# Optimization experiments

Measured on AMD Instinct MI355X. Metric: run time of the kernel, lower is better.

Reference implementation:

```python
import jax, jax.numpy as jnp
import numpy as np

T, B, E = 1024, 4, 1024
H = 16
D = E // H          # head_dim = 64
L = 16              # max_relative_length


def setup_inputs() -> dict:
    key = jax.random.key(0)
    ks = jax.random.split(key, 4)
    query = jax.random.normal(ks[0], (T, B, E), dtype=jnp.float32)
    # xavier-ish scaled params
    in_proj_weight = jax.random.normal(ks[1], (3 * E, E), dtype=jnp.float32) * (1.0 / np.sqrt(E))
    in_proj_bias = jnp.zeros((3 * E,), dtype=jnp.float32)
    rel_pos_keys = jax.random.normal(ks[2], (2 * L + 1, E), dtype=jnp.float32) * (1.0 / np.sqrt(E))
    out_w = jax.random.normal(ks[3], (E, E), dtype=jnp.float32) * (1.0 / np.sqrt(E))
    out_b = jnp.zeros((E,), dtype=jnp.float32)
    return {"query": query, "in_proj_weight": in_proj_weight, "in_proj_bias": in_proj_bias,
            "rel_pos_keys": rel_pos_keys, "out_w": out_w, "out_b": out_b}


def reference(query, in_proj_weight, in_proj_bias, rel_pos_keys, out_w, out_b):
    t, b, e = query.shape
    scaling = D ** (-0.5)
    # fused qkv projection: [T,B,3E]
    qkv = jnp.einsum('tbe,fe->tbf', query, in_proj_weight) + in_proj_bias
    q, k, v = jnp.split(qkv, 3, axis=-1)
    q = q * scaling
    # [T,B,E] -> [B*H, T, D]
    def heads(x):
        return x.reshape(t, b * H, D).transpose(1, 0, 2)
    q, k, v = heads(q), heads(k), heads(v)
    # clipped relative position matrix [T,T] in [0, 2L]
    r = jnp.arange(t)
    dist = jnp.clip(r[None, :] - r[:, None], -L, L) + L
    # gather relation keys, keep first head_dim channels: [T,T,D]
    rel_k = rel_pos_keys[dist][:, :, :D]
    # scores = q k^T + q . rel_k  (Shaw et al.), [B*H, T, T]
    scores = jnp.einsum('btd,bsd->bts', q, k) + jnp.einsum('btd,tsd->bts', q, rel_k)
    probs = jax.nn.softmax(scores, axis=-1)
    attn = jnp.einsum('bts,bsd->btd', probs, v)      # [B*H, T, D]
    attn = attn.transpose(1, 0, 2).reshape(t, b, e)   # [T, B, E]
    return jnp.einsum('tbe,oe->tbo', attn, out_w) + out_b
```

## Files before the change

kernel.cpp:

```cpp
#include <hip/hip_runtime.h>
#include <hip/hip_bf16.h>

typedef __attribute__((ext_vector_type(8))) short short8;
typedef __attribute__((ext_vector_type(4))) float floatx4;


#define QSCALE 0.18033688011112043f

__device__ __forceinline__ short f2bf(float x) {
  union { float f; unsigned u; } cv; cv.f = x;
  unsigned u = cv.u + (0x7FFFu + ((cv.u >> 16) & 1u));
  return (short)(u >> 16);
}

__device__ __forceinline__ unsigned pk_bf16(float a, float b) {
  union { __hip_bfloat162 h; unsigned u; } cv;
  cv.h = __float22bfloat162_rn(make_float2(a, b));
  return cv.u;
}

__device__ __forceinline__ float exp2_hw(float x) {
  return __builtin_amdgcn_exp2f(x);
}

__device__ __forceinline__ floatx4 mfma16(short8 a, short8 b, floatx4 c) {
  return __builtin_amdgcn_mfma_f32_16x16x32_bf16(a, b, c, 0, 0, 0);
}

__device__ __forceinline__ void async_copy16(const void* g, void* l) {
  __builtin_amdgcn_global_load_lds((const __attribute__((address_space(1))) void*)g,
                                   (__attribute__((address_space(3))) void*)l, 16, 0, 0);
}

__global__ void __launch_bounds__(256) convert_all_kernel(
    const float* __restrict__ s0, const float* __restrict__ s1,
    const float* __restrict__ s2,
    short* __restrict__ d0, short* __restrict__ d1, short* __restrict__ d2)
{
  int i = blockIdx.x * 256 + threadIdx.x;
  if (i < 524288) {
    int e8 = i & 127, b = (i >> 7) & 3, t = i >> 9;
    const float4* s = (const float4*)s0 + (size_t)i * 2;
    float4 a = s[0], c = s[1];
    uint4 o = make_uint4(pk_bf16(a.x, a.y), pk_bf16(a.z, a.w),
                         pk_bf16(c.x, c.y), pk_bf16(c.z, c.w));
    *(uint4*)(d0 + (size_t)b * 1048576 + t * 1024 + e8 * 8) = o;
  } else {
    const float* src; short* dst; int off;
    if (i < 917504) { src = s1; dst = d1; off = i - 524288; }
    else            { src = s2; dst = d2; off = i - 917504; }
    const float4* s = (const float4*)src + (size_t)off * 2;
    float4 a = s[0], c = s[1];
    uint4 o = make_uint4(pk_bf16(a.x, a.y), pk_bf16(a.z, a.w),
                         pk_bf16(c.x, c.y), pk_bf16(c.z, c.w));
    *(uint4*)(dst + (size_t)off * 8) = o;
  }
}

__device__ __forceinline__ void gemm_stage(
    const short* __restrict__ A, const short* __restrict__ W,
    short* Atile, short* Btile, int m0, int n0, int K, int kk, int tid, int w)
{
  #pragma unroll
  for (int i = 0; i < 2; i++) {
    int seg = i * 256 + tid;
    int row = seg >> 2, p = seg & 3;
    int ck = (p - ((row >> 1) & 3)) & 3;
    async_copy16(A + (size_t)(m0 + row) * K + kk + ck * 8,
                 Atile + (size_t)(i * 256 + w * 64) * 8);
    async_copy16(W + (size_t)(n0 + row) * K + kk + ck * 8,
                 Btile + (size_t)(i * 256 + w * 64) * 8);
  }
}

__device__ __forceinline__ void gemm_core_db(
    const short* __restrict__ A, const short* __restrict__ W,
    short* At, short* Bt,
    int m0, int n0, int K, int tid, floatx4 acc[4][4])
{
  const int lane = tid & 63, w = tid >> 6;
  const int quad = lane >> 4, l16 = lane & 15;
  const int wm = (w >> 1) * 64, wn = (w & 1) * 64;
  #pragma unroll
  for (int mt = 0; mt < 4; mt++)
    #pragma unroll
    for (int nt = 0; nt < 4; nt++) acc[mt][nt] = (floatx4)(0.0f);

  gemm_stage(A, W, At, Bt, m0, n0, K, 0, tid, w);

  for (int kk = 0; kk < K; kk += 32) {
    const int cur = (kk >> 5) & 1;
    short* Ac = At + cur * (128 * 32);
    short* Bc = Bt + cur * (128 * 32);
    __syncthreads();
    if (kk + 32 < K)
      gemm_stage(A, W, At + (1 - cur) * (128 * 32), Bt + (1 - cur) * (128 * 32),
                 m0, n0, K, kk + 32, tid, w);
    short8 af[4], bfr[4];
    #pragma unroll
    for (int mt = 0; mt < 4; mt++) {
      int R = wm + mt * 16 + l16;
      af[mt] = *(const short8*)(Ac + R * 32 + ((quad + (R >> 1)) & 3) * 8);
    }
    #pragma unroll
    for (int nt = 0; nt < 4; nt++) {
      int R = wn + nt * 16 + l16;
      bfr[nt] = *(const short8*)(Bc + R * 32 + ((quad + (R >> 1)) & 3) * 8);
    }
    #pragma unroll
    for (int mt = 0; mt < 4; mt++)
      #pragma unroll
      for (int nt = 0; nt < 4; nt++)
        acc[mt][nt] = mfma16(af[mt], bfr[nt], acc[mt][nt]);
  }
}

__global__ void __launch_bounds__(256) gemm_qkv(
    const short* __restrict__ A, const short* __restrict__ W,
    const float* __restrict__ bias,
    short* __restrict__ q_ws, short* __restrict__ k_ws, short* __restrict__ v_ws)
{
  __shared__ __align__(16) short Atile[2 * 128 * 32];
  __shared__ __align__(16) short Btile[2 * 128 * 32];
  const int tid = threadIdx.x;
  const int m0 = blockIdx.x * 128, n0 = blockIdx.y * 128;
  floatx4 acc[4][4];
  gemm_core_db(A, W, Atile, Btile, m0, n0, 1024, tid, acc);

  const int lane = tid & 63, w = tid >> 6;
  const int quad = lane >> 4, l16 = lane & 15;
  const int wm = (w >> 1) * 64, wn = (w & 1) * 64;
  const int which = n0 >> 10;
  #pragma unroll
  for (int nt = 0; nt < 4; nt++) {
    int f = n0 + wn + nt * 16 + l16;
    float bv = bias[f];
    int h = (f >> 6) & 15;
    int d = f & 63;
    if (which == 2) {
      #pragma unroll
      for (int mt = 0; mt < 4; mt++) {
        int r0 = m0 + wm + mt * 16 + quad * 4;
        int t = r0 & 1023, bb = r0 >> 10;
        int bh = bb * 16 + h;
        unsigned lo = pk_bf16(acc[mt][nt][0] + bv, acc[mt][nt][1] + bv);
        unsigned hi = pk_bf16(acc[mt][nt][2] + bv, acc[mt][nt][3] + bv);
        *(uint2*)(v_ws + ((size_t)bh * 64 + d) * 1024 + t) = make_uint2(lo, hi);
      }
    } else {
      short* dst = which ? k_ws : q_ws;
      const float sc = which ? 1.0f : QSCALE;
      #pragma unroll
      for (int mt = 0; mt < 4; mt++) {
        int r0 = m0 + wm + mt * 16 + quad * 4;
        int t = r0 & 1023, bb = r0 >> 10;
        int bh = bb * 16 + h;
        unsigned u01 = pk_bf16((acc[mt][nt][0] + bv) * sc, (acc[mt][nt][1] + bv) * sc);
        unsigned u23 = pk_bf16((acc[mt][nt][2] + bv) * sc, (acc[mt][nt][3] + bv) * sc);
        size_t base = ((size_t)bh * 1024 + t) * 64 + d;
        dst[base]           = (short)u01;
        dst[base + 64]      = (short)(u01 >> 16);
        dst[base + 128]     = (short)u23;
        dst[base + 192]     = (short)(u23 >> 16);
      }
    }
  }
}

__global__ void __launch_bounds__(256) attn_kernel(
    const short* __restrict__ q_ws, const short* __restrict__ k_ws,
    const short* __restrict__ v_ws, const float* __restrict__ relk,
    short* __restrict__ attn_ws)
{
  __shared__ float rel_lds[128 * 33];
  __shared__ __align__(16) short Ktile[2][64 * 64];
  __shared__ __align__(16) short Vtile[2][64 * 64];
  __shared__ __align__(16) short p_lds[4][32 * 64];
  const int tid = threadIdx.x, lane = tid & 63, w = tid >> 6;
  const int quad = lane >> 4, l16 = lane & 15;
  const int bh = 8 * ((int)blockIdx.x & 7) + (((int)blockIdx.x >> 3) & 7);
  const int t0 = ((int)blockIdx.x >> 6) * 128;
  const int b = bh >> 4, h = bh & 15;

  short8 aq[2][2];
  #pragma unroll
  for (int qt = 0; qt < 2; qt++)
    #pragma unroll
    for (int ks = 0; ks < 2; ks++)
      aq[qt][ks] = *(const short8*)(q_ws
          + ((size_t)bh * 1024 + t0 + qt * 64 + w * 16 + l16) * 64
          + ks * 32 + quad * 8);

  for (int i = tid; i < 48 * 8; i += 256) {
    int row = i >> 3, p = i & 7;
    short8 val;
    if (row < 33) {
      const float* src = relk + row * 1024 + p * 8;
      float4 a = *(const float4*)src, c = *(const float4*)(src + 4);
      val[0] = f2bf(a.x); val[1] = f2bf(a.y); val[2] = f2bf(a.z); val[3] = f2bf(a.w);
      val[4] = f2bf(c.x); val[5] = f2bf(c.y); val[6] = f2bf(c.z); val[7] = f2bf(c.w);
    } else {
      val = (short8)0;
    }
    *(short8*)(Ktile[0] + row * 64 + ((p ^ (row & 7)) << 3)) = val;
  }
  __syncthreads();

  #pragma unroll
  for (int qt = 0; qt < 2; qt++) {
    #pragma unroll
    for (int jt = 0; jt < 3; jt++) {
      floatx4 scR = (floatx4)(0.0f);
      #pragma unroll
      for (int ks = 0; ks < 2; ks++) {
        int rrow = jt * 16 + l16;
        int ck = (quad + 4 * ks) ^ (rrow & 7);
        short8 rb = *(const short8*)(Ktile[0] + rrow * 64 + ck * 8);
        scR = mfma16(aq[qt][ks], rb, scR);
      }
      int j = jt * 16 + l16;
      if (j < 33) {
        #pragma unroll
        for (int reg = 0; reg < 4; reg++) {
          int tl = qt * 64 + w * 16 + quad * 4 + reg;
          rel_lds[tl * 33 + j] = scR[reg];
        }
      }
    }
  }
  __syncthreads();

  float biasLo[2], biasHi[2];
  #pragma unroll
  for (int qt = 0; qt < 2; qt++) {
    int ql = qt * 64 + w * 16 + l16;
    biasLo[qt] = rel_lds[ql * 33 + 0];
    biasHi[qt] = rel_lds[ql * 33 + 32];
  }

  floatx4 o[2][4];
  #pragma unroll
  for (int qt = 0; qt < 2; qt++)
    #pragma unroll
    for (int dt = 0; dt < 4; dt++) o[qt][dt] = (floatx4)(0.0f);
  float rsum[2] = {0.f, 0.f};

  const short* kg = k_ws + (size_t)bh * 1024 * 64;
  const short* vg = v_ws + (size_t)bh * 64 * 1024;

  #define STAGE_KV(S0, BUF)                                                  \
    {                                                                        \
      _Pragma("unroll")                                                      \
      for (int i = 0; i < 2; i++) {                                          \
        int seg = i * 256 + tid;                                             \
        int row = seg >> 3, p = seg & 7;                                     \
        int ck = p ^ (row & 7);                                              \
        async_copy16(kg + (size_t)((S0) + row) * 64 + ck * 8,                \
                     Ktile[BUF] + (size_t)(i * 256 + w * 64) * 8);           \
        async_copy16(vg + (size_t)row * 1024 + (S0) + ck * 8,                \
                     Vtile[BUF] + (size_t)(i * 256 + w * 64) * 8);           \
      }                                                                      \
    }

  STAGE_KV(0, 0);

  for (int st = 0; st < 16; st++) {
    const int s0 = st * 64;
    const int cur = st & 1;
    __syncthreads();
    if (st < 15) STAGE_KV(s0 + 64, 1 - cur);

    short8 kb[4][2];
    #pragma unroll
    for (int nt = 0; nt < 4; nt++)
      #pragma unroll
      for (int ks = 0; ks < 2; ks++) {
        int srow = nt * 16 + l16;
        kb[nt][ks] = *(const short8*)(Ktile[cur] + srow * 64
                                      + (((quad + 4 * ks) ^ (l16 & 7)) << 3));
      }

    floatx4 sc[2][4];
    #pragma unroll
    for (int qt = 0; qt < 2; qt++)
      #pragma unroll
      for (int nt = 0; nt < 4; nt++) {
        sc[qt][nt] = (floatx4)(0.0f);
        #pragma unroll
        for (int ks = 0; ks < 2; ks++)
          sc[qt][nt] = mfma16(kb[nt][ks], aq[qt][ks], sc[qt][nt]);
      }

    #pragma unroll
    for (int qt = 0; qt < 2; qt++) {
      const int qbase = t0 + qt * 64 + w * 16;
      bool alllo = (s0 <= qbase - 79);
      bool allhi = (s0 >= qbase + 31);
      if (alllo || allhi) {
        float bb = alllo ? biasLo[qt] : biasHi[qt];
        #pragma unroll
        for (int nt = 0; nt < 4; nt++)
          #pragma unroll
          for (int reg = 0; reg < 4; reg++) sc[qt][nt][reg] += bb;
      } else {
        int ql = qt * 64 + w * 16 + l16;
        #pragma unroll
        for (int nt = 0; nt < 4; nt++)
          #pragma unroll
          for (int reg = 0; reg < 4; reg++) {
            int delta = (s0 + 16 * nt + 4 * quad + reg) - (qbase + l16);
            delta = min(max(delta, -16), 16) + 16;
            sc[qt][nt][reg] += rel_lds[ql * 33 + delta];
          }
      }
      #pragma unroll
      for (int nt = 0; nt < 4; nt++) {
        #pragma unroll
        for (int reg = 0; reg < 4; reg++) {
          float p = exp2_hw(sc[qt][nt][reg]);
          sc[qt][nt][reg] = p;
          rsum[qt] += p;
        }
        unsigned w0 = pk_bf16(sc[qt][nt][0], sc[qt][nt][1]);
        unsigned w1 = pk_bf16(sc[qt][nt][2], sc[qt][nt][3]);
        int srot = (16 * nt + 4 * quad + 4 * l16) & 63;
        *(uint2*)(p_lds[w] + (qt * 16 + l16) * 64 + srot) = make_uint2(w0, w1);
      }
    }

    short8 ap[2][2];
    #pragma unroll
    for (int qt = 0; qt < 2; qt++)
      #pragma unroll
      for (int ks = 0; ks < 2; ks++) {
        int s1 = (32 * ks + 8 * quad + 4 * l16) & 63;
        int s2 = (s1 + 4) & 63;
        union { short8 v; uint2 u[2]; } pu;
        pu.u[0] = *(const uint2*)(p_lds[w] + (qt * 16 + l16) * 64 + s1);
        pu.u[1] = *(const uint2*)(p_lds[w] + (qt * 16 + l16) * 64 + s2);
        ap[qt][ks] = pu.v;
      }

    #pragma unroll
    for (int dt = 0; dt < 4; dt++) {
      short8 vb[2];
      #pragma unroll
      for (int ks = 0; ks < 2; ks++) {
        int drow = dt * 16 + l16;
        vb[ks] = *(const short8*)(Vtile[cur] + drow * 64
                                  + (((quad + 4 * ks) ^ (l16 & 7)) << 3));
      }
      #pragma unroll
      for (int qt = 0; qt < 2; qt++)
        #pragma unroll
        for (int ks = 0; ks < 2; ks++)
          o[qt][dt] = mfma16(ap[qt][ks], vb[ks], o[qt][dt]);
    }
  }
  #undef STAGE_KV

  #pragma unroll
  for (int qt = 0; qt < 2; qt++) {
    float rs = rsum[qt];
    rs += __shfl_xor(rs, 16, 64);
    rs += __shfl_xor(rs, 32, 64);
    float inv[4];
    #pragma unroll
    for (int reg = 0; reg < 4; reg++)
      inv[reg] = 1.0f / __shfl(rs, quad * 4 + reg, 64);
    #pragma unroll
    for (int dt = 0; dt < 4; dt++) {
      unsigned u01 = pk_bf16(o[qt][dt][0] * inv[0], o[qt][dt][1] * inv[1]);
      unsigned u23 = pk_bf16(o[qt][dt][2] * inv[2], o[qt][dt][3] * inv[3]);
      int tg = t0 + qt * 64 + w * 16 + quad * 4;
      size_t base = ((size_t)tg * 4 + b) * 1024 + h * 64 + dt * 16 + l16;
      attn_ws[base]         = (short)u01;
      attn_ws[base + 4096]  = (short)(u01 >> 16);
      attn_ws[base + 8192]  = (short)u23;
      attn_ws[base + 12288] = (short)(u23 >> 16);
    }
  }
}

__global__ void __launch_bounds__(256) gemm_outproj(
    const short* __restrict__ A, const short* __restrict__ W,
    const float* __restrict__ bias, float* __restrict__ out)
{
  __shared__ __align__(16) short Atile[2 * 64 * 32];
  __shared__ __align__(16) short Btile[2 * 128 * 32];
  const int tid = threadIdx.x;
  const int m0 = blockIdx.x * 64, n0 = blockIdx.y * 128;
  const int lane = tid & 63, w = tid >> 6;
  const int quad = lane >> 4, l16 = lane & 15;
  const int wm = (w >> 1) * 32, wn = (w & 1) * 64;

  floatx4 acc[2][4];
  #pragma unroll
  for (int mt = 0; mt < 2; mt++)
    #pragma unroll
    for (int nt = 0; nt < 4; nt++) acc[mt][nt] = (floatx4)(0.0f);

  #define STAGE_OP(KK, BUF)                                                  \
    {                                                                        \
      _Pragma("unroll")                                                      \
      for (int i = 0; i < 2; i++) {                                          \
        int seg = i * 256 + tid;                \
        int row = seg >> 2, p = seg & 3;                                     \
        int ck = (p - ((row >> 1) & 3)) & 3;                                 \
        async_copy16(W + (size_t)(n0 + row) * 1024 + (KK) + ck * 8,          \
                     Btile + (size_t)((BUF) * 4096 + (i * 256 + w * 64) * 8)); \
      }                                                                      \
      {                                                                      \
        int row = tid >> 2, p = tid & 3;         \
        int ck = (p - ((row >> 1) & 3)) & 3;                                 \
        async_copy16(A + (size_t)(m0 + row) * 1024 + (KK) + ck * 8,          \
                     Atile + (size_t)((BUF) * 2048 + (w * 64) * 8));         \
      }                                                                      \
    }

  STAGE_OP(0, 0);
  for (int kk = 0; kk < 1024; kk += 32) {
    const int cur = (kk >> 5) & 1;
    const short* Ac = Atile + cur * 2048;
    const short* Bc = Btile + cur * 4096;
    __syncthreads();
    if (kk + 32 < 1024) STAGE_OP(kk + 32, 1 - cur);
    short8 af[2], bfr[4];
    #pragma unroll
    for (int mt = 0; mt < 2; mt++) {
      int R = wm + mt * 16 + l16;
      af[mt] = *(const short8*)(Ac + R * 32 + ((quad + (R >> 1)) & 3) * 8);
    }
    #pragma unroll
    for (int nt = 0; nt < 4; nt++) {
      int R = wn + nt * 16 + l16;
      bfr[nt] = *(const short8*)(Bc + R * 32 + ((quad + (R >> 1)) & 3) * 8);
    }
    #pragma unroll
    for (int mt = 0; mt < 2; mt++)
      #pragma unroll
      for (int nt = 0; nt < 4; nt++)
        acc[mt][nt] = mfma16(af[mt], bfr[nt], acc[mt][nt]);
  }
  #undef STAGE_OP

  #pragma unroll
  for (int nt = 0; nt < 4; nt++) {
    int f = n0 + wn + nt * 16 + l16;
    float bv = bias[f];
    #pragma unroll
    for (int mt = 0; mt < 2; mt++) {
      #pragma unroll
      for (int reg = 0; reg < 4; reg++) {
        int r = m0 + wm + mt * 16 + quad * 4 + reg;
        out[(size_t)r * 1024 + f] = acc[mt][nt][reg] + bv;
      }
    }
  }
}

extern "C" void kernel_launch(void* const* d_in, const int* in_sizes, int n_in,
                              void* d_out, int out_size, void* d_ws, size_t ws_size,
                              hipStream_t stream) {
  const float* query = (const float*)d_in[0];
  const float* in_w  = (const float*)d_in[1];
  const float* in_b  = (const float*)d_in[2];
  const float* relk  = (const float*)d_in[3];
  const float* out_w = (const float*)d_in[4];
  const float* out_b = (const float*)d_in[5];
  float* out = (float*)d_out;

  short* qry_bf = (short*)d_ws;
  short* win_bf = qry_bf + (size_t)4096 * 1024;
  short* wout_bf = win_bf + (size_t)3072 * 1024;
  short* q_ws   = wout_bf + (size_t)1024 * 1024;
  short* k_ws   = q_ws + (size_t)64 * 1024 * 64;
  short* v_ws   = k_ws + (size_t)64 * 1024 * 64;
  short* att_ws = v_ws + (size_t)64 * 1024 * 64;

  convert_all_kernel<<<4096, 256, 0, stream>>>(query, in_w, out_w,
                                               qry_bf, win_bf, wout_bf);
  gemm_qkv<<<dim3(32, 24), 256, 0, stream>>>(qry_bf, win_bf, in_b, q_ws, k_ws, v_ws);
  attn_kernel<<<512, 256, 0, stream>>>(q_ws, k_ws, v_ws, relk, att_ws);
  gemm_outproj<<<dim3(64, 8), 256, 0, stream>>>(att_ws, wout_bf, out_b, out);
}
```

Baseline: 175.4 us.

## Rewrite QKV GEMM with 256x256 tiles and ping-pong scheduled MFMA phases

The QKV projection GEMM moves from 128x128 tiles with 4 waves and K=32 stages to 256x256 tiles with 8 waves and K=64 stages. It uses XOR-swizzled LDS and a four-phase schedule per k-step that interleaves LDS fragment reads, async global loads and MFMA bursts. Barriers, sched_barrier and setprio pin that ordering. The aim is more data reuse per load and overlapping memory traffic with matrix math. The grid drops to 192 blocks, which leaves some CUs idle and uses much more LDS per block.

```diff
diff --git a/kernel.cpp b/kernel.cpp
--- a/kernel.cpp
+++ b/kernel.cpp
@@ -57,79 +57,162 @@
   }
 }
 
-__device__ __forceinline__ void gemm_stage(
-    const short* __restrict__ A, const short* __restrict__ W,
-    short* Atile, short* Btile, int m0, int n0, int K, int kk, int tid, int w)
-{
+__device__ __forceinline__ void stage_half8(const short* __restrict__ g,
+                                            short* l, int tid, int w) {
   #pragma unroll
   for (int i = 0; i < 2; i++) {
-    int seg = i * 256 + tid;
-    int row = seg >> 2, p = seg & 3;
-    int ck = (p - ((row >> 1) & 3)) & 3;
-    async_copy16(A + (size_t)(m0 + row) * K + kk + ck * 8,
-                 Atile + (size_t)(i * 256 + w * 64) * 8);
-    async_copy16(W + (size_t)(n0 + row) * K + kk + ck * 8,
-                 Btile + (size_t)(i * 256 + w * 64) * 8);
-  }
-}
-
-__device__ __forceinline__ void gemm_core_db(
-    const short* __restrict__ A, const short* __restrict__ W,
-    short* At, short* Bt,
-    int m0, int n0, int K, int tid, floatx4 acc[4][4])
-{
-  const int lane = tid & 63, w = tid >> 6;
-  const int quad = lane >> 4, l16 = lane & 15;
-  const int wm = (w >> 1) * 64, wn = (w & 1) * 64;
-  #pragma unroll
-  for (int mt = 0; mt < 4; mt++)
-    #pragma unroll
-    for (int nt = 0; nt < 4; nt++) acc[mt][nt] = (floatx4)(0.0f);
-
-  gemm_stage(A, W, At, Bt, m0, n0, K, 0, tid, w);
-
-  for (int kk = 0; kk < K; kk += 32) {
-    const int cur = (kk >> 5) & 1;
-    short* Ac = At + cur * (128 * 32);
-    short* Bc = Bt + cur * (128 * 32);
-    __syncthreads();
-    if (kk + 32 < K)
-      gemm_stage(A, W, At + (1 - cur) * (128 * 32), Bt + (1 - cur) * (128 * 32),
-                 m0, n0, K, kk + 32, tid, w);
-    short8 af[4], bfr[4];
-    #pragma unroll
-    for (int mt = 0; mt < 4; mt++) {
-      int R = wm + mt * 16 + l16;
-      af[mt] = *(const short8*)(Ac + R * 32 + ((quad + (R >> 1)) & 3) * 8);
-    }
-    #pragma unroll
-    for (int nt = 0; nt < 4; nt++) {
-      int R = wn + nt * 16 + l16;
-      bfr[nt] = *(const short8*)(Bc + R * 32 + ((quad + (R >> 1)) & 3) * 8);
-    }
-    #pragma unroll
-    for (int mt = 0; mt < 4; mt++)
-      #pragma unroll
-      for (int nt = 0; nt < 4; nt++)
-        acc[mt][nt] = mfma16(af[mt], bfr[nt], acc[mt][nt]);
-  }
-}
-
-__global__ void __launch_bounds__(256) gemm_qkv(
+    int seg = i * 512 + tid;
+    int row = seg >> 3, p = seg & 7;
+    int ck = p ^ (row & 7);
+    async_copy16(g + (size_t)row * 1024 + ck * 8,
+                 l + (size_t)(i * 512 + w * 64) * 8);
+  }
+}
+
+__global__ void __launch_bounds__(512, 2) gemm_qkv(
     const short* __restrict__ A, const short* __restrict__ W,
     const float* __restrict__ bias,
     short* __restrict__ q_ws, short* __restrict__ k_ws, short* __restrict__ v_ws)
 {
-  __shared__ __align__(16) short Atile[2 * 128 * 32];
-  __shared__ __align__(16) short Btile[2 * 128 * 32];
-  const int tid = threadIdx.x;
-  const int m0 = blockIdx.x * 128, n0 = blockIdx.y * 128;
-  floatx4 acc[4][4];
-  gemm_core_db(A, W, Atile, Btile, m0, n0, 1024, tid, acc);
-
-  const int lane = tid & 63, w = tid >> 6;
+  __shared__ __align__(16) short Atile[2 * 2 * 128 * 64];
+  __shared__ __align__(16) short Btile[2 * 2 * 128 * 64];
+  const int tid = threadIdx.x, lane = tid & 63, w = tid >> 6;
   const int quad = lane >> 4, l16 = lane & 15;
-  const int wm = (w >> 1) * 64, wn = (w & 1) * 64;
+  const int m0 = blockIdx.x * 256, n0 = blockIdx.y * 256;
+  const int wm = (w >> 2) * 128, wn = (w & 3) * 64;
+  const int rowB0 = (w & 1) * 64;
+
+  const short* Ag = A + (size_t)m0 * 1024;
+  const short* Wg = W + (size_t)n0 * 1024;
+
+  floatx4 acc[8][4];
+  #pragma unroll
+  for (int mt = 0; mt < 8; mt++)
+    #pragma unroll
+    for (int nt = 0; nt < 4; nt++) acc[mt][nt] = (floatx4)(0.0f);
+
+  #define SH_A(kc, h, buf) stage_half8(Ag + (size_t)(h) * 131072 + (kc) * 64, \
+                                       Atile + (buf) * 16384 + (h) * 8192, tid, w)
+  #define SH_B(kc, h, buf) stage_half8(Wg + (size_t)(h) * 131072 + (kc) * 64, \
+                                       Btile + (buf) * 16384 + (h) * 8192, tid, w)
+
+  SH_A(0, 0, 0); SH_A(0, 1, 0); SH_B(0, 0, 0); SH_B(0, 1, 0);
+  SH_A(1, 0, 1); SH_A(1, 1, 1);
+  asm volatile("s_waitcnt vmcnt(4)" ::: "memory");
+  __builtin_amdgcn_s_barrier();
+  asm volatile("" ::: "memory");
+
+  for (int kt = 0; kt < 16; ++kt) {
+    const int cur = kt & 1, nxt = cur ^ 1;
+    const short* Ah = Atile + cur * 16384 + (w >> 2) * 8192;
+    const short* Bh = Btile + cur * 16384 + ((w & 3) >> 1) * 8192;
+    const int kc1 = (kt + 1 < 16) ? kt + 1 : 15;
+    const int kc2 = (kt + 2 < 16) ? kt + 2 : 15;
+
+    short8 alo[4][2], ahi[4][2], blo[2][2], bhi[2][2];
+
+    #pragma unroll
+    for (int mt = 0; mt < 4; mt++) {
+      int r = mt * 16 + l16;
+      #pragma unroll
+      for (int ks = 0; ks < 2; ks++)
+        alo[mt][ks] = *(const short8*)(Ah + r * 64 + (((quad + 4 * ks) ^ (r & 7)) << 3));
+    }
+    #pragma unroll
+    for (int nt = 0; nt < 2; nt++) {
+      int r = rowB0 + nt * 16 + l16;
+      #pragma unroll
+      for (int ks = 0; ks < 2; ks++)
+        blo[nt][ks] = *(const short8*)(Bh + r * 64 + (((quad + 4 * ks) ^ (r & 7)) << 3));
+    }
+    SH_B(kc1, 0, nxt);
+    asm volatile("" ::: "memory");
+    __builtin_amdgcn_s_barrier();
+    __builtin_amdgcn_sched_barrier(0);
+    __builtin_amdgcn_s_setprio(1);
+    #pragma unroll
+    for (int mt = 0; mt < 4; mt++)
+      #pragma unroll
+      for (int nt = 0; nt < 2; nt++)
+        #pragma unroll
+        for (int ks = 0; ks < 2; ks++)
+          acc[mt][nt] = mfma16(alo[mt][ks], blo[nt][ks], acc[mt][nt]);
+    __builtin_amdgcn_s_setprio(0);
+    __builtin_amdgcn_sched_barrier(0);
+    __builtin_amdgcn_s_barrier();
+    asm volatile("" ::: "memory");
+
+    #pragma unroll
+    for (int mt = 0; mt < 4; mt++) {
+      int r = 64 + mt * 16 + l16;
+      #pragma unroll
+      for (int ks = 0; ks < 2; ks++)
+        ahi[mt][ks] = *(const short8*)(Ah + r * 64 + (((quad + 4 * ks) ^ (r & 7)) << 3));
+    }
+    SH_B(kc1, 1, nxt);
+    asm volatile("" ::: "memory");
+    __builtin_amdgcn_s_barrier();
+    __builtin_amdgcn_sched_barrier(0);
+    __builtin_amdgcn_s_setprio(1);
+    #pragma unroll
+    for (int mt = 0; mt < 4; mt++)
+      #pragma unroll
+      for (int nt = 0; nt < 2; nt++)
+        #pragma unroll
+        for (int ks = 0; ks < 2; ks++)
+          acc[4 + mt][nt] = mfma16(ahi[mt][ks], blo[nt][ks], acc[4 + mt][nt]);
+    __builtin_amdgcn_s_setprio(0);
+    __builtin_amdgcn_sched_barrier(0);
+    __builtin_amdgcn_s_barrier();
+    asm volatile("" ::: "memory");
+
+    #pragma unroll
+    for (int nt = 0; nt < 2; nt++) {
+      int r = rowB0 + (2 + nt) * 16 + l16;
+      #pragma unroll
+      for (int ks = 0; ks < 2; ks++)
+        bhi[nt][ks] = *(const short8*)(Bh + r * 64 + (((quad + 4 * ks) ^ (r & 7)) << 3));
+    }
+    SH_A(kc2, 0, cur);
+    asm volatile("" ::: "memory");
+    __builtin_amdgcn_s_barrier();
+    __builtin_amdgcn_sched_barrier(0);
+    __builtin_amdgcn_s_setprio(1);
+    #pragma unroll
+    for (int mt = 0; mt < 4; mt++)
+      #pragma unroll
+      for (int nt = 0; nt < 2; nt++)
+        #pragma unroll
+        for (int ks = 0; ks < 2; ks++)
+          acc[4 + mt][2 + nt] = mfma16(ahi[mt][ks], bhi[nt][ks], acc[4 + mt][2 + nt]);
+    __builtin_amdgcn_s_setprio(0);
+    __builtin_amdgcn_sched_barrier(0);
+    __builtin_amdgcn_s_barrier();
+    asm volatile("" ::: "memory");
+
+    SH_A(kc2, 1, cur);
+    asm volatile("s_waitcnt vmcnt(4)" ::: "memory");
+    asm volatile("" ::: "memory");
+    __builtin_amdgcn_s_barrier();
+    __builtin_amdgcn_sched_barrier(0);
+    __builtin_amdgcn_s_setprio(1);
+    #pragma unroll
+    for (int mt = 0; mt < 4; mt++)
+      #pragma unroll
+      for (int nt = 0; nt < 2; nt++)
+        #pragma unroll
+        for (int ks = 0; ks < 2; ks++)
+          acc[mt][2 + nt] = mfma16(alo[mt][ks], bhi[nt][ks], acc[mt][2 + nt]);
+    __builtin_amdgcn_s_setprio(0);
+    __builtin_amdgcn_sched_barrier(0);
+    __builtin_amdgcn_s_barrier();
+    asm volatile("" ::: "memory");
+  }
+  #undef SH_A
+  #undef SH_B
+
+  asm volatile("s_waitcnt vmcnt(0)" ::: "memory");
+
   const int which = n0 >> 10;
   #pragma unroll
   for (int nt = 0; nt < 4; nt++) {
@@ -139,7 +222,7 @@
     int d = f & 63;
     if (which == 2) {
       #pragma unroll
-      for (int mt = 0; mt < 4; mt++) {
+      for (int mt = 0; mt < 8; mt++) {
         int r0 = m0 + wm + mt * 16 + quad * 4;
         int t = r0 & 1023, bb = r0 >> 10;
         int bh = bb * 16 + h;
@@ -151,7 +234,7 @@
       short* dst = which ? k_ws : q_ws;
       const float sc = which ? 1.0f : QSCALE;
       #pragma unroll
-      for (int mt = 0; mt < 4; mt++) {
+      for (int mt = 0; mt < 8; mt++) {
         int r0 = m0 + wm + mt * 16 + quad * 4;
         int t = r0 & 1023, bb = r0 >> 10;
         int bh = bb * 16 + h;
@@ -480,7 +563,7 @@
 
   convert_all_kernel<<<4096, 256, 0, stream>>>(query, in_w, out_w,
                                                qry_bf, win_bf, wout_bf);
-  gemm_qkv<<<dim3(32, 24), 256, 0, stream>>>(qry_bf, win_bf, in_b, q_ws, k_ws, v_ws);
+  gemm_qkv<<<dim3(16, 12), 512, 0, stream>>>(qry_bf, win_bf, in_b, q_ws, k_ws, v_ws);
   attn_kernel<<<512, 256, 0, stream>>>(q_ws, k_ws, v_ws, relk, att_ws);
   gemm_outproj<<<dim3(64, 8), 256, 0, stream>>>(att_ws, wout_bf, out_b, out);
 }
```

New measurement: 178.1 us. Within noise of the previous version (+1.6%).

## Retile QKV GEMM to 256x192 tiles with 512 threads and BK=64

Applied to the files above, without the earlier changes.

Rewrites the QKV projection GEMM to use 256x192 output tiles, K-chunks of 64 with XOR-swizzled LDS, 8 waves per block, and loads fragments before issuing the next stage's async copies. This raises per-block data reuse and MFMA density and gives 256 blocks, a closer match to the CU count. It also adds s_setprio around MFMA sections in both the GEMM and the attention kernel to favor matrix issue. The cost is a larger LDS footprint and more accumulator registers, which may limit occupancy.

```diff
diff --git a/kernel.cpp b/kernel.cpp
--- a/kernel.cpp
+++ b/kernel.cpp
@@ -57,90 +57,108 @@
   }
 }
 
-__device__ __forceinline__ void gemm_stage(
-    const short* __restrict__ A, const short* __restrict__ W,
-    short* Atile, short* Btile, int m0, int n0, int K, int kk, int tid, int w)
-{
-  #pragma unroll
-  for (int i = 0; i < 2; i++) {
-    int seg = i * 256 + tid;
-    int row = seg >> 2, p = seg & 3;
-    int ck = (p - ((row >> 1) & 3)) & 3;
-    async_copy16(A + (size_t)(m0 + row) * K + kk + ck * 8,
-                 Atile + (size_t)(i * 256 + w * 64) * 8);
-    async_copy16(W + (size_t)(n0 + row) * K + kk + ck * 8,
-                 Btile + (size_t)(i * 256 + w * 64) * 8);
-  }
-}
-
-__device__ __forceinline__ void gemm_core_db(
-    const short* __restrict__ A, const short* __restrict__ W,
-    short* At, short* Bt,
-    int m0, int n0, int K, int tid, floatx4 acc[4][4])
-{
-  const int lane = tid & 63, w = tid >> 6;
-  const int quad = lane >> 4, l16 = lane & 15;
-  const int wm = (w >> 1) * 64, wn = (w & 1) * 64;
-  #pragma unroll
-  for (int mt = 0; mt < 4; mt++)
-    #pragma unroll
-    for (int nt = 0; nt < 4; nt++) acc[mt][nt] = (floatx4)(0.0f);
-
-  gemm_stage(A, W, At, Bt, m0, n0, K, 0, tid, w);
-
-  for (int kk = 0; kk < K; kk += 32) {
-    const int cur = (kk >> 5) & 1;
-    short* Ac = At + cur * (128 * 32);
-    short* Bc = Bt + cur * (128 * 32);
-    __syncthreads();
-    if (kk + 32 < K)
-      gemm_stage(A, W, At + (1 - cur) * (128 * 32), Bt + (1 - cur) * (128 * 32),
-                 m0, n0, K, kk + 32, tid, w);
-    short8 af[4], bfr[4];
-    #pragma unroll
-    for (int mt = 0; mt < 4; mt++) {
-      int R = wm + mt * 16 + l16;
-      af[mt] = *(const short8*)(Ac + R * 32 + ((quad + (R >> 1)) & 3) * 8);
-    }
-    #pragma unroll
-    for (int nt = 0; nt < 4; nt++) {
-      int R = wn + nt * 16 + l16;
-      bfr[nt] = *(const short8*)(Bc + R * 32 + ((quad + (R >> 1)) & 3) * 8);
-    }
-    #pragma unroll
-    for (int mt = 0; mt < 4; mt++)
-      #pragma unroll
-      for (int nt = 0; nt < 4; nt++)
-        acc[mt][nt] = mfma16(af[mt], bfr[nt], acc[mt][nt]);
-  }
-}
-
-__global__ void __launch_bounds__(256) gemm_qkv(
+__global__ void __launch_bounds__(512, 2) gemm_qkv(
     const short* __restrict__ A, const short* __restrict__ W,
     const float* __restrict__ bias,
     short* __restrict__ q_ws, short* __restrict__ k_ws, short* __restrict__ v_ws)
 {
-  __shared__ __align__(16) short Atile[2 * 128 * 32];
-  __shared__ __align__(16) short Btile[2 * 128 * 32];
-  const int tid = threadIdx.x;
-  const int m0 = blockIdx.x * 128, n0 = blockIdx.y * 128;
-  floatx4 acc[4][4];
-  gemm_core_db(A, W, Atile, Btile, m0, n0, 1024, tid, acc);
-
-  const int lane = tid & 63, w = tid >> 6;
+  __shared__ __align__(16) short Atile[2 * 256 * 64];
+  __shared__ __align__(16) short Btile[2 * 192 * 64];
+  const int tid = threadIdx.x, lane = tid & 63, w = tid >> 6;
   const int quad = lane >> 4, l16 = lane & 15;
-  const int wm = (w >> 1) * 64, wn = (w & 1) * 64;
-  const int which = n0 >> 10;
-  #pragma unroll
-  for (int nt = 0; nt < 4; nt++) {
+  const int m0 = blockIdx.x * 256, n0 = blockIdx.y * 192;
+  const int wmh = (w >> 2);
+  const int wn = (w & 3) * 48;
+
+  const short* Ag = A + (size_t)m0 * 1024;
+  const short* Wg = W + (size_t)n0 * 1024;
+
+  floatx4 acc[8][3];
+  #pragma unroll
+  for (int mt = 0; mt < 8; mt++)
+    #pragma unroll
+    for (int nt = 0; nt < 3; nt++) acc[mt][nt] = (floatx4)(0.0f);
+
+  #define STAGE_A(kc, buf)                                                   \
+    {                                                                        \
+      _Pragma("unroll")                                                      \
+      for (int i = 0; i < 4; i++) {                                          \
+        int seg = i * 512 + tid;                                             \
+        int row = seg >> 3, p = seg & 7;                                     \
+        int ck = p ^ (row & 7);                                              \
+        async_copy16(Ag + (size_t)row * 1024 + (kc) * 64 + ck * 8,           \
+                     Atile + (buf) * 16384 + (size_t)(i * 512 + w * 64) * 8);\
+      }                                                                      \
+    }
+  #define STAGE_B(kc, buf)                                                   \
+    {                                                                        \
+      _Pragma("unroll")                                                      \
+      for (int i = 0; i < 3; i++) {                                          \
+        int seg = i * 512 + tid;                                             \
+        int row = seg >> 3, p = seg & 7;                                     \
+        int ck = p ^ (row & 7);                                              \
+        async_copy16(Wg + (size_t)row * 1024 + (kc) * 64 + ck * 8,           \
+                     Btile + (buf) * 12288 + (size_t)(i * 512 + w * 64) * 8);\
+      }                                                                      \
+    }
+
+  STAGE_A(0, 0); STAGE_B(0, 0);
+  asm volatile("s_waitcnt vmcnt(0)" ::: "memory");
+  __builtin_amdgcn_s_barrier();
+
+  for (int kt = 0; kt < 16; ++kt) {
+    const int cur = kt & 1, nxt = cur ^ 1;
+    const int kc1 = (kt + 1 < 16) ? kt + 1 : 15;
+
+    short8 af[8][2], bf[3][2];
+    #pragma unroll
+    for (int mt = 0; mt < 8; mt++) {
+      int r = mt * 16 + l16;
+      int gr = wmh * 128 + r;
+      #pragma unroll
+      for (int ks = 0; ks < 2; ks++)
+        af[mt][ks] = *(const short8*)(Atile + cur * 16384 + gr * 64
+                                      + (((quad + 4 * ks) ^ (r & 7)) << 3));
+    }
+    #pragma unroll
+    for (int nt = 0; nt < 3; nt++) {
+      int row = wn + nt * 16 + l16;
+      #pragma unroll
+      for (int ks = 0; ks < 2; ks++)
+        bf[nt][ks] = *(const short8*)(Btile + cur * 12288 + row * 64
+                                      + (((quad + 4 * ks) ^ (row & 7)) << 3));
+    }
+
+    STAGE_A(kc1, nxt); STAGE_B(kc1, nxt);
+
+    __builtin_amdgcn_s_setprio(1);
+    #pragma unroll
+    for (int mt = 0; mt < 8; mt++)
+      #pragma unroll
+      for (int nt = 0; nt < 3; nt++)
+        #pragma unroll
+        for (int ks = 0; ks < 2; ks++)
+          acc[mt][nt] = mfma16(af[mt][ks], bf[nt][ks], acc[mt][nt]);
+    __builtin_amdgcn_s_setprio(0);
+    __builtin_amdgcn_sched_barrier(0);
+
+    asm volatile("s_waitcnt vmcnt(0)" ::: "memory");
+    __builtin_amdgcn_s_barrier();
+  }
+  #undef STAGE_A
+  #undef STAGE_B
+
+  #pragma unroll
+  for (int nt = 0; nt < 3; nt++) {
     int f = n0 + wn + nt * 16 + l16;
     float bv = bias[f];
+    int which = f >> 10;
     int h = (f >> 6) & 15;
     int d = f & 63;
     if (which == 2) {
       #pragma unroll
-      for (int mt = 0; mt < 4; mt++) {
-        int r0 = m0 + wm + mt * 16 + quad * 4;
+      for (int mt = 0; mt < 8; mt++) {
+        int r0 = m0 + wmh * 128 + mt * 16 + quad * 4;
         int t = r0 & 1023, bb = r0 >> 10;
         int bh = bb * 16 + h;
         unsigned lo = pk_bf16(acc[mt][nt][0] + bv, acc[mt][nt][1] + bv);
@@ -151,8 +169,8 @@
       short* dst = which ? k_ws : q_ws;
       const float sc = which ? 1.0f : QSCALE;
       #pragma unroll
-      for (int mt = 0; mt < 4; mt++) {
-        int r0 = m0 + wm + mt * 16 + quad * 4;
+      for (int mt = 0; mt < 8; mt++) {
+        int r0 = m0 + wmh * 128 + mt * 16 + quad * 4;
         int t = r0 & 1023, bb = r0 >> 10;
         int bh = bb * 16 + h;
         unsigned u01 = pk_bf16((acc[mt][nt][0] + bv) * sc, (acc[mt][nt][1] + bv) * sc);
@@ -281,6 +299,7 @@
       }
 
     floatx4 sc[2][4];
+    __builtin_amdgcn_s_setprio(1);
     #pragma unroll
     for (int qt = 0; qt < 2; qt++)
       #pragma unroll
@@ -290,6 +309,7 @@
         for (int ks = 0; ks < 2; ks++)
           sc[qt][nt] = mfma16(kb[nt][ks], aq[qt][ks], sc[qt][nt]);
       }
+    __builtin_amdgcn_s_setprio(0);
 
     #pragma unroll
     for (int qt = 0; qt < 2; qt++) {
@@ -341,6 +361,7 @@
         ap[qt][ks] = pu.v;
       }
 
+    __builtin_amdgcn_s_setprio(1);
     #pragma unroll
     for (int dt = 0; dt < 4; dt++) {
       short8 vb[2];
@@ -356,6 +377,7 @@
         for (int ks = 0; ks < 2; ks++)
           o[qt][dt] = mfma16(ap[qt][ks], vb[ks], o[qt][dt]);
     }
+    __builtin_amdgcn_s_setprio(0);
   }
   #undef STAGE_KV
 
@@ -480,7 +502,7 @@
 
   convert_all_kernel<<<4096, 256, 0, stream>>>(query, in_w, out_w,
                                                qry_bf, win_bf, wout_bf);
-  gemm_qkv<<<dim3(32, 24), 256, 0, stream>>>(qry_bf, win_bf, in_b, q_ws, k_ws, v_ws);
+  gemm_qkv<<<dim3(16, 16), 512, 0, stream>>>(qry_bf, win_bf, in_b, q_ws, k_ws, v_ws);
   attn_kernel<<<512, 256, 0, stream>>>(q_ws, k_ws, v_ws, relk, att_ws);
   gemm_outproj<<<dim3(64, 8), 256, 0, stream>>>(att_ws, wout_bf, out_b, out);
 }
```

After: 168.3 us. 4.0% less time.
